# Kernel tuning notes

Hardware: AMD Instinct MI355X
Metric: run time of the kernel (lower is better)

Reference implementation:

```python
import jax, jax.numpy as jnp
import numpy as np

B, T, H, NH = 4, 2048, 1024, 16
HD = H // NH  # 64


def setup_inputs() -> dict:
    key = jax.random.key(0)
    ks = jax.random.split(key, 8)
    s = 1.0 / np.sqrt(H)
    return {
        "hidden_states": jax.random.normal(ks[0], (B, T, H), dtype=jnp.float32),
        "attention_mask": jnp.zeros((B, 1, 1, T), dtype=jnp.float32),
        "Wq": jax.random.normal(ks[1], (H, H), dtype=jnp.float32) * s,
        "bq": jax.random.normal(ks[2], (H,), dtype=jnp.float32) * 0.01,
        "Wk": jax.random.normal(ks[3], (H, H), dtype=jnp.float32) * s,
        "bk": jax.random.normal(ks[4], (H,), dtype=jnp.float32) * 0.01,
        "Wv": jax.random.normal(ks[5], (H, H), dtype=jnp.float32) * s,
        "bv": jax.random.normal(ks[6], (H,), dtype=jnp.float32) * 0.01,
    }


def _split_heads(x):
    # [b, t, h*d] -> [b, h, t, d]
    b, t, _ = x.shape
    return x.reshape(b, t, NH, HD).transpose(0, 2, 1, 3)


def reference(hidden_states, attention_mask, Wq, bq, Wk, bk, Wv, bv):
    q = _split_heads(hidden_states @ Wq.T + bq)
    k = _split_heads(hidden_states @ Wk.T + bk)
    v = _split_heads(hidden_states @ Wv.T + bv)
    scores = jnp.einsum('bhqd,bhkd->bhqk', q, k) / jnp.sqrt(jnp.float32(HD))
    t = q.shape[2]
    causal = jnp.triu(jnp.ones((t, t), dtype=scores.dtype), k=1)[None, None] * (-1e9)
    scores = scores + causal + attention_mask
    probs = jax.nn.softmax(scores, axis=-1)
    # module returns [b, h, t, d] (no merge back)
    return jnp.einsum('bhqk,bhkd->bhqd', probs, v)
```

## Files before the change

### kernel.cpp

```cpp
#include <hip/hip_runtime.h>
#include <hip/hip_bf16.h>


typedef float  f32x4 __attribute__((ext_vector_type(4)));
typedef short  s16x8 __attribute__((ext_vector_type(8)));
typedef unsigned short u16;

#define LOG2E 1.44269504088896340736f

__device__ __forceinline__ u16 f2bf(float f) {
  unsigned u = __float_as_uint(f);
  u += 0x7FFFu + ((u >> 16) & 1u);
  return (u16)(u >> 16);
}
__device__ __forceinline__ float bf2f(u16 v) {
  return __uint_as_float(((unsigned)v) << 16);
}
__device__ __forceinline__ float ex2(float x) {
#if __has_builtin(__builtin_amdgcn_exp2f)
  return __builtin_amdgcn_exp2f(x);
#else
  return exp2f(x);
#endif
}
__device__ __forceinline__ float rcp_(float x) {
#if __has_builtin(__builtin_amdgcn_rcpf)
  return __builtin_amdgcn_rcpf(x);
#else
  return 1.0f / x;
#endif
}
__device__ __forceinline__ unsigned cvtpk(float lo, float hi) {
  unsigned r;
  asm("v_cvt_pk_bf16_f32 %0, %1, %2" : "=v"(r) : "v"(lo), "v"(hi));
  return r;
}
__device__ __forceinline__ void bar() {
  asm volatile("" ::: "memory");
  __builtin_amdgcn_s_barrier();
  asm volatile("" ::: "memory");
}

#define GLOAD16(gp, lp)                                                          \
  __builtin_amdgcn_global_load_lds(                                              \
      (const __attribute__((address_space(1))) void*)(gp),                       \
      (__attribute__((address_space(3))) void*)(lp), 16, 0, 0)

#define MFMA(a, b, c) __builtin_amdgcn_mfma_f32_16x16x32_bf16((a), (b), (c), 0, 0, 0)

__global__ __launch_bounds__(256) void cvt_all(
    const float* __restrict__ hs, const float* __restrict__ wq,
    const float* __restrict__ wk, const float* __restrict__ wv,
    const float* __restrict__ maskp,
    u16* __restrict__ xo, u16* __restrict__ qo, u16* __restrict__ ko,
    u16* __restrict__ vo, u16* __restrict__ wm) {
  int b = blockIdx.x;
  const float* s;
  u16* d;
  size_t i;
  bool isw = false;
  if (b < 4096) { s = hs; d = xo; i = (size_t)b * 256 + threadIdx.x; }
  else if (b < 5632) {
    int w = (b - 4096) >> 9, r = (b - 4096) & 511;
    s = (w == 0) ? wq : (w == 1) ? wk : wv;
    d = (w == 0) ? qo : (w == 1) ? ko : vo;
    i = (size_t)r * 256 + threadIdx.x;
  } else {
    s = maskp; d = wm; i = (size_t)(b - 5632) * 256 + threadIdx.x;
    isw = true;
  }
  const float4* sp = (const float4*)s + i * 2;
  float4 a = sp[0], c = sp[1];
  s16x8 r8;
  if (isw) {
    r8[0] = f2bf(ex2(a.x * LOG2E)); r8[1] = f2bf(ex2(a.y * LOG2E));
    r8[2] = f2bf(ex2(a.z * LOG2E)); r8[3] = f2bf(ex2(a.w * LOG2E));
    r8[4] = f2bf(ex2(c.x * LOG2E)); r8[5] = f2bf(ex2(c.y * LOG2E));
    r8[6] = f2bf(ex2(c.z * LOG2E)); r8[7] = f2bf(ex2(c.w * LOG2E));
  } else {
    r8[0] = f2bf(a.x); r8[1] = f2bf(a.y); r8[2] = f2bf(a.z); r8[3] = f2bf(a.w);
    r8[4] = f2bf(c.x); r8[5] = f2bf(c.y); r8[6] = f2bf(c.z); r8[7] = f2bf(c.w);
  }
  *(s16x8*)(d + i * 8) = r8;
}

__global__ __launch_bounds__(256, 2) void qkv_gemm(
    const u16* __restrict__ Xb,
    const u16* __restrict__ Wqb, const u16* __restrict__ Wkb,
    const u16* __restrict__ Wvb,
    const float* __restrict__ bq, const float* __restrict__ bk,
    const float* __restrict__ bv, const u16* __restrict__ Wm,
    u16* __restrict__ Qo, u16* __restrict__ Ko, u16* __restrict__ Vto) {
  int bid0 = blockIdx.x;
  int bid  = (bid0 & 7) * 96 + (bid0 >> 3);
  int which = bid % 3;
  int rt = bid / 3;
  int mt = rt >> 3, nt = rt & 7;
  const u16* W = (which == 0) ? Wqb : (which == 1) ? Wkb : Wvb;
  const float* bias = (which == 0) ? bq : (which == 1) ? bk : bv;

  __shared__ __align__(16) char lds[49152];

  int tid = threadIdx.x;
  int lane = tid & 63, wid = tid >> 6;
  int q16 = lane & 15, g = lane >> 4;
  int wr = wid >> 1, wc = wid & 1;

  int srow = tid >> 2;
  int sw = (((tid & 3) ^ ((srow >> 1) & 3)) << 4);
  const char* Asrc = (const char*)Xb + (size_t)(mt * 256 + srow) * 2048 + sw;
  const char* Bsrc = (const char*)W  + (size_t)(nt * 128 + srow) * 2048 + sw;

  int slotA = (g ^ ((q16 >> 1) & 3)) << 4;

#define STAGE_AB(tt, buf) do { size_t so = (size_t)(tt) * 64;                    \
    GLOAD16(Asrc + so,          lds + (buf) * 16384 + tid * 16);                 \
    GLOAD16(Asrc + so + 131072, lds + (buf) * 16384 + 4096 + tid * 16);          \
    GLOAD16(Asrc + so + 262144, lds + (buf) * 16384 + 8192 + tid * 16);          \
    GLOAD16(Asrc + so + 393216, lds + (buf) * 16384 + 12288 + tid * 16);         \
    GLOAD16(Bsrc + so,          lds + 32768 + (buf) * 8192 + tid * 16);          \
    GLOAD16(Bsrc + so + 131072, lds + 32768 + (buf) * 8192 + 4096 + tid * 16); } while (0)

  STAGE_AB(0, 0);

  f32x4 acc[8][4] = {};
  s16x8 fA[8], fB[4];

#pragma unroll 1
  for (int i = 0; i < 32; ++i) {
    int buf = i & 1;
    if (i < 31) {
      STAGE_AB(i + 1, buf ^ 1);
      asm volatile("s_waitcnt vmcnt(6)" ::: "memory");
    } else {
      asm volatile("s_waitcnt vmcnt(0)" ::: "memory");
    }
    bar();
    const char* pa = lds + buf * 16384 + (wr * 128 + q16) * 64 + slotA;
    const char* pb = lds + 32768 + buf * 8192 + (wc * 64 + q16) * 64 + slotA;
#pragma unroll
    for (int m = 0; m < 8; ++m) fA[m] = *(const s16x8*)(pa + m * 1024);
#pragma unroll
    for (int n = 0; n < 4; ++n) fB[n] = *(const s16x8*)(pb + n * 1024);
    __builtin_amdgcn_s_setprio(1);
#pragma unroll
    for (int m = 0; m < 8; ++m)
#pragma unroll
      for (int n = 0; n < 4; ++n)
        acc[m][n] = MFMA(fA[m], fB[n], acc[m][n]);
    __builtin_amdgcn_s_setprio(0);
    bar();
  }
#undef STAGE_AB

  float qsc = (which == 0) ? (0.125f * LOG2E) : 1.0f;
  u16* Out = (which == 0) ? Qo : (which == 1) ? Ko : Vto;
  int h0 = nt * 2 + wc;
  u16* tile = (u16*)(void*)(lds + wid * 12288);
  const char* tb = (const char*)tile;
  int rl = lane >> 3, cb = (lane & 7) * 16;

#define EPIPASS(P) do {                                                          \
    int mbase = mt * 256 + wr * 128 + (P) * 64;                                  \
    int bb = mbase >> 11, t0 = mbase & 2047;                                     \
    if (which != 2) {                                                            \
      _Pragma("unroll")                                                          \
      for (int n = 0; n < 4; ++n) {                                              \
        float bvl = bias[h0 * 64 + n * 16 + q16];                                \
        _Pragma("unroll")                                                        \
        for (int mm = 0; mm < 4; ++mm)                                           \
          _Pragma("unroll")                                                      \
          for (int j = 0; j < 4; ++j)                                            \
            tile[(mm * 16 + g * 4 + j) * 72 + n * 16 + q16] =                    \
                f2bf((acc[(P) * 4 + mm][n][j] + bvl) * qsc);                     \
      }                                                                          \
    } else {                                                                     \
      const u16* wrow = Wm + (size_t)bb * 2048 + t0;                             \
      float wv[4][4];                                                            \
      _Pragma("unroll")                                                          \
      for (int mm = 0; mm < 4; ++mm)                                             \
        _Pragma("unroll")                                                        \
        for (int j = 0; j < 4; ++j)                                              \
          wv[mm][j] = bf2f(wrow[mm * 16 + g * 4 + j]);                           \
      _Pragma("unroll")                                                          \
      for (int n = 0; n < 4; ++n) {                                              \
        float bvl = bias[h0 * 64 + n * 16 + q16];                                \
        _Pragma("unroll")                                                        \
        for (int mm = 0; mm < 4; ++mm)                                           \
          _Pragma("unroll")                                                      \
          for (int j = 0; j < 4; ++j)                                            \
            tile[(n * 16 + q16) * 72 + mm * 16 + g * 4 + j] =                    \
                f2bf((acc[(P) * 4 + mm][n][j] + bvl) * wv[mm][j]);               \
      }                                                                          \
    }                                                                            \
    asm volatile("" ::: "memory");                                               \
    if (which != 2) {                                                            \
      char* gbase = (char*)(Out + ((size_t)(bb * 16 + h0) * 2048 + t0) * 64);    \
      _Pragma("unroll")                                                          \
      for (int c = 0; c < 8; ++c) {                                              \
        int row = rl + c * 8;                                                    \
        s16x8 v = *(const s16x8*)(tb + row * 144 + cb);                          \
        *(s16x8*)(gbase + row * 128 + cb) = v;                                   \
      }                                                                          \
    } else {                                                                     \
      char* gbase = (char*)Out + ((size_t)(bb * 16 + h0) * 64) * 4096 + t0 * 2;  \
      _Pragma("unroll")                                                          \
      for (int c = 0; c < 8; ++c) {                                              \
        int d = rl + c * 8;                                                      \
        s16x8 v = *(const s16x8*)(tb + d * 144 + cb);                            \
        *(s16x8*)(gbase + (size_t)d * 4096 + cb) = v;                            \
      }                                                                          \
    }                                                                            \
    asm volatile("" ::: "memory"); } while (0)

  EPIPASS(0);
  EPIPASS(1);
#undef EPIPASS
}

__global__ __launch_bounds__(256, 2) void attn_fwd(
    const u16* __restrict__ Qw, const u16* __restrict__ Kw,
    const u16* __restrict__ Vtw, const u16* __restrict__ Wm,
    float* __restrict__ out) {
  int bid0 = blockIdx.x;
  int bid = (bid0 & 7) * 64 + (bid0 >> 3);
  int bh = bid >> 3, p = bid & 7;
  int tid = threadIdx.x;
  int lane = tid & 63, wid = tid >> 6;
  int q16 = lane & 15, g = lane >> 4;

  __shared__ __align__(16) char Ks[4][8192];
  __shared__ __align__(16) char Vs[4][8192];
  __shared__ __align__(16) u16 wl[2048];

  int srow = tid >> 3;
  int sinner = (tid & 7) << 4;
  int fs = (srow & 7) ^ ((srow >> 1) & 4);
  int ssw = sinner ^ (fs << 4);
  const char* Kg = (const char*)Kw + ((size_t)bh * 2048 + srow) * 128 + ssw;
  const char* Vg = (const char*)Vtw + ((size_t)bh * 64 + srow) * 4096 + ssw;

#define STAGE_T(kt, b) do {                                                      \
    GLOAD16(Kg + (size_t)(kt) * 8192,        Ks[b] + tid * 16);                  \
    GLOAD16(Kg + (size_t)(kt) * 8192 + 4096, Ks[b] + tid * 16 + 4096);           \
    GLOAD16(Vg + (size_t)(kt) * 128,          Vs[b] + tid * 16);                 \
    GLOAD16(Vg + (size_t)(kt) * 128 + 131072, Vs[b] + tid * 16 + 4096); } while (0)

  GLOAD16((const char*)Wm + (size_t)(bh >> 4) * 4096 + tid * 16,
          (char*)wl + tid * 16);

  auto run_phase = [&](int qtl) {
    int nt = 2 * qtl + 2;
    int qw0 = (qtl << 7) + wid * 32;
    size_t qr = (size_t)bh * 2048 + qw0 + q16;
    s16x8 qa[2][2];
#pragma unroll
    for (int h = 0; h < 2; ++h) {
      qa[h][0] = *(const s16x8*)(Qw + (qr + 16 * h) * 64 + g * 8);
      qa[h][1] = *(const s16x8*)(Qw + (qr + 16 * h) * 64 + 32 + g * 8);
    }
    bar();
    STAGE_T(0, 0);
    STAGE_T(1, 1);

    f32x4 o[2][4] = {};
    f32x4 lw[2] = {};

#pragma unroll 1
    for (int kt = 0; kt < nt; ++kt) {
      if (kt + 2 < nt) {
        STAGE_T(kt + 2, (kt + 2) & 3);
        asm volatile("s_waitcnt vmcnt(8)" ::: "memory");
      } else if (kt + 1 < nt) {
        asm volatile("s_waitcnt vmcnt(4)" ::: "memory");
      } else {
        asm volatile("s_waitcnt vmcnt(0)" ::: "memory");
      }
      bar();

      if (64 * kt <= qw0 + 31) {
        int kb = kt << 6;
        const char* ksb = Ks[kt & 3];
        const char* vsb = Vs[kt & 3];
        bool causal = (64 * kt + 63 > qw0);
#pragma unroll
        for (int c = 0; c < 2; ++c) {
          f32x4 sA[2][2];
          __builtin_amdgcn_s_setprio(1);
#pragma unroll
          for (int t4 = 0; t4 < 2; ++t4) {
            int kk = 32 * c + ((q16 >> 2) << 3) + (t4 << 2) + (q16 & 3);
            int fk = (kk & 7) ^ ((kk >> 1) & 4);
            const char* krow = ksb + kk * 128;
            int in0 = (g * 16) ^ (fk << 4);
            s16x8 kf0 = *(const s16x8*)(krow + in0);
            s16x8 kf1 = *(const s16x8*)(krow + (in0 ^ 64));
#pragma unroll
            for (int h = 0; h < 2; ++h) {
              f32x4 sv = {0.f, 0.f, 0.f, 0.f};
              sv = MFMA(kf0, qa[h][0], sv);
              sv = MFMA(kf1, qa[h][1], sv);
              sA[t4][h] = sv;
            }
          }
          __builtin_amdgcn_s_setprio(0);

          s16x8 wf = *(const s16x8*)((const char*)wl + (kb + 32 * c + 8 * g) * 2);

          union { s16x8 v; unsigned u[4]; } pb[2];
#pragma unroll
          for (int h = 0; h < 2; ++h) {
            int qc = qw0 + 16 * h + q16;
#pragma unroll
            for (int t4 = 0; t4 < 2; ++t4) {
              float a0 = ex2(sA[t4][h][0]), a1 = ex2(sA[t4][h][1]);
              float a2 = ex2(sA[t4][h][2]), a3 = ex2(sA[t4][h][3]);
              if (causal) {
                int k0 = kb + 32 * c + 8 * g + 4 * t4;
                a0 = (k0 + 0 <= qc) ? a0 : 0.f;
                a1 = (k0 + 1 <= qc) ? a1 : 0.f;
                a2 = (k0 + 2 <= qc) ? a2 : 0.f;
                a3 = (k0 + 3 <= qc) ? a3 : 0.f;
              }
              pb[h].u[t4 * 2 + 0] = cvtpk(a0, a1);
              pb[h].u[t4 * 2 + 1] = cvtpk(a2, a3);
            }
          }

          __builtin_amdgcn_s_setprio(1);
#pragma unroll
          for (int dt = 0; dt < 4; ++dt) {
            int d = dt * 16 + q16;
            int fv = (d & 7) ^ ((d >> 1) & 4);
            s16x8 vf = *(const s16x8*)(vsb + d * 128 + ((64 * c + 16 * g) ^ (fv << 4)));
#pragma unroll
            for (int h = 0; h < 2; ++h)
              o[h][dt] = MFMA(vf, pb[h].v, o[h][dt]);
          }
#pragma unroll
          for (int h = 0; h < 2; ++h)
            lw[h] = MFMA(wf, pb[h].v, lw[h]);
          __builtin_amdgcn_s_setprio(0);
        }
      }
    }

#pragma unroll
    for (int h = 0; h < 2; ++h) {
      float inv = rcp_(lw[h][0]);
      float* op = out + ((size_t)bh * 2048 + qw0 + 16 * h + q16) * 64 + g * 4;
#pragma unroll
      for (int dt = 0; dt < 4; ++dt)
        *(f32x4*)(op + dt * 16) = o[h][dt] * inv;
    }
  };

  run_phase(15 - p);
  run_phase(p);
#undef STAGE_T
}

extern "C" void kernel_launch(void* const* d_in, const int* in_sizes, int n_in,
                              void* d_out, int out_size, void* d_ws, size_t ws_size,
                              hipStream_t stream) {
  const float* hs   = (const float*)d_in[0];
  const float* mask = (const float*)d_in[1];
  const float* Wq   = (const float*)d_in[2];
  const float* bq   = (const float*)d_in[3];
  const float* Wk   = (const float*)d_in[4];
  const float* bk   = (const float*)d_in[5];
  const float* Wv   = (const float*)d_in[6];
  const float* bv   = (const float*)d_in[7];
  float* out = (float*)d_out;

  char* w = (char*)d_ws;
  u16* Xb  = (u16*)w; w += (size_t)8192 * 1024 * 2;
  u16* Wqb = (u16*)w; w += (size_t)1024 * 1024 * 2;
  u16* Wkb = (u16*)w; w += (size_t)1024 * 1024 * 2;
  u16* Wvb = (u16*)w; w += (size_t)1024 * 1024 * 2;
  u16* Qw  = (u16*)w; w += (size_t)8192 * 1024 * 2;
  u16* Kw  = (u16*)w; w += (size_t)8192 * 1024 * 2;
  u16* Vtw = (u16*)w; w += (size_t)8192 * 1024 * 2;
  u16* Wm  = (u16*)w; w += (size_t)8192 * 2;

  cvt_all<<<5636, 256, 0, stream>>>(hs, Wq, Wk, Wv, mask, Xb, Wqb, Wkb, Wvb, Wm);
  qkv_gemm<<<768, 256, 0, stream>>>(Xb, Wqb, Wkb, Wvb, bq, bk, bv, Wm, Qw, Kw, Vtw);
  attn_fwd<<<512, 256, 0, stream>>>(Qw, Kw, Vtw, Wm, out);
}
```

Baseline: 129.5 us.

## Load B operand directly from global into registers, unroll K loop by two

In the QKV projection GEMM, the weight (B) tiles are now read straight from global memory into register fragments with double-buffered register sets, instead of being staged through LDS. Only the activation (A) tile still goes through LDS. The K loop is unrolled by two so LDS and register buffers alternate with fixed indices. This cuts LDS traffic and LDS reads for B. The cost is more VGPR pressure and uncoalesced direct global loads, since each lane reads 16 bytes from rows 2 KB apart, and the vmcnt accounting must match the mixed load types.

```diff
diff --git a/kernel.cpp b/kernel.cpp
--- a/kernel.cpp
+++ b/kernel.cpp
@@ -109,49 +109,69 @@
   int srow = tid >> 2;
   int sw = (((tid & 3) ^ ((srow >> 1) & 3)) << 4);
   const char* Asrc = (const char*)Xb + (size_t)(mt * 256 + srow) * 2048 + sw;
-  const char* Bsrc = (const char*)W  + (size_t)(nt * 128 + srow) * 2048 + sw;
+
+  const char* Bgc = (const char*)W + (size_t)(nt * 128 + wc * 64 + q16) * 2048 + g * 16;
 
   int slotA = (g ^ ((q16 >> 1) & 3)) << 4;
 
-#define STAGE_AB(tt, buf) do { size_t so = (size_t)(tt) * 64;                    \
+#define STAGE_A(tt, buf) do { size_t so = (size_t)(tt) * 64;                     \
     GLOAD16(Asrc + so,          lds + (buf) * 16384 + tid * 16);                 \
     GLOAD16(Asrc + so + 131072, lds + (buf) * 16384 + 4096 + tid * 16);          \
     GLOAD16(Asrc + so + 262144, lds + (buf) * 16384 + 8192 + tid * 16);          \
-    GLOAD16(Asrc + so + 393216, lds + (buf) * 16384 + 12288 + tid * 16);         \
-    GLOAD16(Bsrc + so,          lds + 32768 + (buf) * 8192 + tid * 16);          \
-    GLOAD16(Bsrc + so + 131072, lds + 32768 + (buf) * 8192 + 4096 + tid * 16); } while (0)
-
-  STAGE_AB(0, 0);
+    GLOAD16(Asrc + so + 393216, lds + (buf) * 16384 + 12288 + tid * 16); } while (0)
+
+#define LOADB(FB, tt) do {                                                       \
+    const char* pb_ = Bgc + (size_t)(tt) * 64;                                   \
+    FB[0] = *(const s16x8*)(pb_);                                                \
+    FB[1] = *(const s16x8*)(pb_ + 16 * 2048);                                    \
+    FB[2] = *(const s16x8*)(pb_ + 32 * 2048);                                    \
+    FB[3] = *(const s16x8*)(pb_ + 48 * 2048); } while (0)
+
+#define LDA8(buf) do {                                                           \
+    const char* pa_ = lds + (buf) * 16384 + (wr * 128 + q16) * 64 + slotA;       \
+    _Pragma("unroll")                                                            \
+    for (int m_ = 0; m_ < 8; ++m_) fA[m_] = *(const s16x8*)(pa_ + m_ * 1024); } while (0)
+
+#define MM32(FB) do {                                                            \
+    __builtin_amdgcn_s_setprio(1);                                               \
+    _Pragma("unroll")                                                            \
+    for (int m_ = 0; m_ < 8; ++m_)                                               \
+      _Pragma("unroll")                                                          \
+      for (int n_ = 0; n_ < 4; ++n_)                                             \
+        acc[m_][n_] = MFMA(fA[m_], FB[n_], acc[m_][n_]);                         \
+    __builtin_amdgcn_s_setprio(0); } while (0)
+
+  STAGE_A(0, 0);
+  s16x8 fBa[4], fBb[4], fA[8];
+  LOADB(fBa, 0);
 
   f32x4 acc[8][4] = {};
-  s16x8 fA[8], fB[4];
 
 #pragma unroll 1
-  for (int i = 0; i < 32; ++i) {
-    int buf = i & 1;
-    if (i < 31) {
-      STAGE_AB(i + 1, buf ^ 1);
-      asm volatile("s_waitcnt vmcnt(6)" ::: "memory");
+  for (int t = 0; t < 16; ++t) {
+    STAGE_A(2 * t + 1, 1);
+    LOADB(fBb, 2 * t + 1);
+    asm volatile("s_waitcnt vmcnt(8)" ::: "memory");
+    bar();
+    LDA8(0);
+    MM32(fBa);
+    bar();
+    if (t < 15) {
+      STAGE_A(2 * t + 2, 0);
+      LOADB(fBa, 2 * t + 2);
+      asm volatile("s_waitcnt vmcnt(8)" ::: "memory");
     } else {
       asm volatile("s_waitcnt vmcnt(0)" ::: "memory");
     }
     bar();
-    const char* pa = lds + buf * 16384 + (wr * 128 + q16) * 64 + slotA;
-    const char* pb = lds + 32768 + buf * 8192 + (wc * 64 + q16) * 64 + slotA;
-#pragma unroll
-    for (int m = 0; m < 8; ++m) fA[m] = *(const s16x8*)(pa + m * 1024);
-#pragma unroll
-    for (int n = 0; n < 4; ++n) fB[n] = *(const s16x8*)(pb + n * 1024);
-    __builtin_amdgcn_s_setprio(1);
-#pragma unroll
-    for (int m = 0; m < 8; ++m)
-#pragma unroll
-      for (int n = 0; n < 4; ++n)
-        acc[m][n] = MFMA(fA[m], fB[n], acc[m][n]);
-    __builtin_amdgcn_s_setprio(0);
+    LDA8(1);
+    MM32(fBb);
     bar();
   }
-#undef STAGE_AB
+#undef STAGE_A
+#undef LOADB
+#undef LDA8
+#undef MM32
 
   float qsc = (which == 0) ? (0.125f * LOG2E) : 1.0f;
   u16* Out = (which == 0) ? Qo : (which == 1) ? Ko : Vto;
```

Result: slower. 159.5 us (+23.2%).
